# Kernel tuning notes

Measured on AMD Instinct MI355X. Metric: run time of the kernel, lower is better.

Reference implementation:

```python
import jax, jax.numpy as jnp
import numpy as np

N_NODES = 100000
N_EDGES = 1250000
IN_DIM = 64
HID_DIM = 64
OUT_DIM = 64
NEG_SLOPE = 0.2
EPS = 1e-16  # PyG softmax denominator epsilon


def _xavier(key, shape):
    fan_in, fan_out = shape[1], shape[0]
    lim = jnp.sqrt(6.0 / (fan_in + fan_out))
    return jax.random.uniform(key, shape, jnp.float32, -lim, lim)


def setup_inputs() -> dict:
    key = jax.random.key(0)
    ks = jax.random.split(key, 10)
    x = jax.random.normal(ks[0], (N_NODES, IN_DIM), jnp.float32)
    edge_index = jax.random.randint(ks[1], (2, N_EDGES), 0, N_NODES, jnp.int64)
    edge_attr = jax.random.uniform(ks[2], (N_EDGES,), jnp.float32)
    # layer 1 params (torch Linear weight layout: [out, in])
    W1 = _xavier(ks[3], (HID_DIM, IN_DIM))
    a_src1 = _xavier(ks[4], (1, HID_DIM))[0]
    a_dst1 = _xavier(ks[5], (1, HID_DIM))[0]
    # layer 2 params
    W2 = _xavier(ks[6], (OUT_DIM, HID_DIM))
    a_src2 = _xavier(ks[7], (1, OUT_DIM))[0]
    a_dst2 = _xavier(ks[8], (1, OUT_DIM))[0]
    return {"x": x, "edge_index": edge_index, "edge_attr": edge_attr,
            "W1": W1, "a_src1": a_src1, "a_dst1": a_dst1,
            "W2": W2, "a_src2": a_src2, "a_dst2": a_dst2}


def gat_layer(x, W, a_src, a_dst, src, dst, edge_weight, num_nodes):
    # linear (no bias): h = x @ W^T, h: [N, out]
    h = x @ W.T
    s_src = h @ a_src  # [N]
    s_dst = h @ a_dst  # [N]
    # per-edge raw score; note j = edge_index[0] (src), i = edge_index[1] (dst)
    alpha = s_src[src] + s_dst[dst]  # [E]
    alpha = jnp.where(alpha >= 0, alpha, NEG_SLOPE * alpha)  # leaky_relu
    # segment softmax over destination nodes
    seg_max = jax.ops.segment_max(alpha, dst, num_segments=num_nodes)
    alpha = jnp.exp(alpha - seg_max[dst])
    seg_sum = jax.ops.segment_sum(alpha, dst, num_segments=num_nodes)
    alpha = alpha / (seg_sum[dst] + EPS)
    alpha = alpha * edge_weight
    # weighted scatter-add aggregation of source features
    msg = h[src] * alpha[:, None]  # [E, out]
    return jax.ops.segment_sum(msg, dst, num_segments=num_nodes)


def reference(x, edge_index, edge_attr, W1, a_src1, a_dst1, W2, a_src2, a_dst2):
    src = edge_index[0]
    dst = edge_index[1]
    h = gat_layer(x, W1, a_src1, a_dst1, src, dst, edge_attr, N_NODES)
    h = jax.nn.relu(h)
    out = gat_layer(h, W2, a_src2, a_dst2, src, dst, edge_attr, N_NODES)
    return out
```

## Files before the change

### kernel.cpp

```cpp
#include <hip/hip_runtime.h>

#define NN 100000
#define NE 1250000
#define DIM 64

#define BSHIFT 8
#define BNODES (1 << BSHIFT)
#define NBUCK ((NN + BNODES - 1) / BNODES)
#define BIN_BLOCKS 256
#define BIN_CHUNK ((NE + BIN_BLOCKS - 1) / BIN_BLOCKS)
#define BCAP 4096

typedef unsigned short bf16_t;
typedef __attribute__((ext_vector_type(8))) short short8;
typedef __attribute__((ext_vector_type(8))) unsigned short ushort8;
typedef __attribute__((ext_vector_type(4))) float f32x4;

static __device__ __forceinline__ bf16_t f2bf(float f) {
    union { float f; unsigned int u; } c; c.f = f;
    unsigned int u = c.u;
    u += 0x7FFFu + ((u >> 16) & 1u);
    return (bf16_t)(u >> 16);
}
static __device__ __forceinline__ float bf2f(bf16_t b) {
    union { unsigned int u; float f; } c; c.u = ((unsigned int)b) << 16;
    return c.f;
}

union ABFrag { short8 v; short s[8]; };

template<bool IN_BF16, bool RELU_IN>
static __device__ __forceinline__
void linear_body(int bid, const void* __restrict__ xin,
                 const float* __restrict__ W,
                 const float* __restrict__ a_src,
                 const float* __restrict__ a_dst,
                 bf16_t* __restrict__ h,
                 float* __restrict__ s_src,
                 float* __restrict__ s_dst)
{
    int tid  = threadIdx.x;
    int lane = tid & 63;
    int wid  = tid >> 6;
    int lr   = lane & 15;
    int lg   = lane >> 4;
    int rowbase = bid * 128 + wid * 16;

    ABFrag Bf[4][2];
#pragma unroll
    for (int t = 0; t < 4; ++t)
#pragma unroll
    for (int s = 0; s < 2; ++s) {
        const f32x4* wp = reinterpret_cast<const f32x4*>(W + (lr + 16*t)*DIM + 32*s + 8*lg);
        f32x4 w0 = wp[0], w1 = wp[1];
#pragma unroll
        for (int j = 0; j < 4; ++j) {
            Bf[t][s].s[j]     = (short)f2bf(w0[j]);
            Bf[t][s].s[j + 4] = (short)f2bf(w1[j]);
        }
    }

    int arow = rowbase + lr;
    if (arow > NN - 1) arow = NN - 1;

    ABFrag Af[2];
    if (IN_BF16) {
        const bf16_t* xp = (const bf16_t*)xin + (size_t)arow * DIM + 8*lg;
#pragma unroll
        for (int s = 0; s < 2; ++s) {
            ushort8 xv = *reinterpret_cast<const ushort8*>(xp + 32*s);
#pragma unroll
            for (int j = 0; j < 8; ++j) {
                unsigned short b = xv[j];
                if (RELU_IN) b = (b & 0x8000u) ? (unsigned short)0 : b;
                Af[s].s[j] = (short)b;
            }
        }
    } else {
        const float* xp = (const float*)xin + (size_t)arow * DIM + 8*lg;
#pragma unroll
        for (int s = 0; s < 2; ++s) {
            const f32x4* xq = reinterpret_cast<const f32x4*>(xp + 32*s);
            f32x4 x0 = xq[0], x1 = xq[1];
#pragma unroll
            for (int j = 0; j < 4; ++j) {
                float f0 = x0[j], f1 = x1[j];
                if (RELU_IN) { f0 = f0 > 0.f ? f0 : 0.f; f1 = f1 > 0.f ? f1 : 0.f; }
                Af[s].s[j]     = (short)f2bf(f0);
                Af[s].s[j + 4] = (short)f2bf(f1);
            }
        }
    }

    f32x4 acc[4] = {{0.f,0.f,0.f,0.f},{0.f,0.f,0.f,0.f},{0.f,0.f,0.f,0.f},{0.f,0.f,0.f,0.f}};
#pragma unroll
    for (int s = 0; s < 2; ++s)
#pragma unroll
    for (int t = 0; t < 4; ++t)
        acc[t] = __builtin_amdgcn_mfma_f32_16x16x32_bf16(Af[s].v, Bf[t][s].v, acc[t], 0, 0, 0);

    float av[4], dv[4];
#pragma unroll
    for (int t = 0; t < 4; ++t) { av[t] = a_src[lr + 16*t]; dv[t] = a_dst[lr + 16*t]; }

    float ssv[4], sdv[4];
#pragma unroll
    for (int r = 0; r < 4; ++r) {
        int row = rowbase + 4*lg + r;
        bool ok = row < NN;
        float ps = 0.f, pd = 0.f;
#pragma unroll
        for (int t = 0; t < 4; ++t) {
            float v = acc[t][r];
            ps += v * av[t];
            pd += v * dv[t];
            if (ok) h[(size_t)row * DIM + lr + 16*t] = f2bf(v);
        }
#pragma unroll
        for (int off = 8; off; off >>= 1) {
            ps += __shfl_xor(ps, off, 64);
            pd += __shfl_xor(pd, off, 64);
        }
        ssv[r] = ps; sdv[r] = pd;
    }
    if (lr == 0) {
#pragma unroll
        for (int r = 0; r < 4; ++r) {
            int row = rowbase + 4*lg + r;
            if (row < NN) { s_src[row] = ssv[r]; s_dst[row] = sdv[r]; }
        }
    }
}

__global__ __launch_bounds__(512)
void bin_hist(const int* __restrict__ dst, int* __restrict__ gcnt)
{
    __shared__ int cnt[NBUCK];
    int tid = threadIdx.x;
    for (int i = tid; i < NBUCK; i += 512) cnt[i] = 0;
    __syncthreads();
    int lo = blockIdx.x * BIN_CHUNK;
    int hi = lo + BIN_CHUNK; if (hi > NE) hi = NE;
    for (int e = lo + tid; e < hi; e += 512)
        atomicAdd(&cnt[dst[e] >> BSHIFT], 1);
    __syncthreads();
    for (int i = tid; i < NBUCK; i += 512)
        gcnt[i * BIN_BLOCKS + blockIdx.x] = cnt[i];
}

__global__ __launch_bounds__(256)
void row_scan(int* __restrict__ gcnt, int* __restrict__ btot)
{
    __shared__ int wpart[4];
    int b    = blockIdx.x;
    int tid  = threadIdx.x;
    int lane = tid & 63;
    int v = gcnt[b * BIN_BLOCKS + tid];
    int sc = v;
#pragma unroll
    for (int off = 1; off <= 32; off <<= 1) {
        int t = __shfl_up(sc, off, 64);
        if (lane >= off) sc += t;
    }
    if (lane == 63) wpart[tid >> 6] = sc;
    __syncthreads();
    if (tid == 0) {
        int run = 0;
#pragma unroll
        for (int k = 0; k < 4; ++k) { int t = wpart[k]; wpart[k] = run; run += t; }
    }
    __syncthreads();
    int incl = sc + wpart[tid >> 6];
    gcnt[b * BIN_BLOCKS + tid] = incl - v;
    if (tid == BIN_BLOCKS - 1) btot[b] = incl;
}

__global__ __launch_bounds__(512)
void scatter_linear1(const int* __restrict__ src, const int* __restrict__ dst,
                     const float* __restrict__ ea,
                     const int* __restrict__ gcnt, const int* __restrict__ btot,
                     int2* __restrict__ region,
                     const float* __restrict__ x, const float* __restrict__ W1,
                     const float* __restrict__ as1, const float* __restrict__ ad1,
                     bf16_t* __restrict__ h,
                     float* __restrict__ ssrc, float* __restrict__ sdst)
{
    if (blockIdx.x < BIN_BLOCKS) {
        __shared__ int2 sbuf[BIN_CHUNK];
        __shared__ unsigned short sbkt[BIN_CHUNK];
        __shared__ int lcur[NBUCK];
        __shared__ int gout[NBUCK];
        __shared__ int wpart[8];
        int tid  = threadIdx.x;
        int lane = tid & 63;
        int blk  = blockIdx.x;

        int cntb = 0, gex = 0;
        if (tid < NBUCK) {
            gex = gcnt[tid * BIN_BLOCKS + blk];
            int nxt = (blk + 1 < BIN_BLOCKS) ? gcnt[tid * BIN_BLOCKS + blk + 1] : btot[tid];
            cntb = nxt - gex;
        }
        int sc = cntb;
#pragma unroll
        for (int off = 1; off <= 32; off <<= 1) {
            int t = __shfl_up(sc, off, 64);
            if (lane >= off) sc += t;
        }
        if (lane == 63) wpart[tid >> 6] = sc;
        __syncthreads();
        if (tid == 0) {
            int run = 0;
#pragma unroll
            for (int k = 0; k < 8; ++k) { int t = wpart[k]; wpart[k] = run; run += t; }
        }
        __syncthreads();
        int excl = sc - cntb + wpart[tid >> 6];
        if (tid < NBUCK) {
            lcur[tid] = excl;
            gout[tid] = tid * BCAP + gex - excl;
        }
        __syncthreads();

        int lo = blk * BIN_CHUNK;
        int hi = lo + BIN_CHUNK; if (hi > NE) hi = NE;
        for (int e = lo + tid; e < hi; e += 512) {
            int d = dst[e];
            int b = d >> BSHIFT;
            int pos = atomicAdd(&lcur[b], 1);
            sbuf[pos] = make_int2(src[e] | ((d & (BNODES - 1)) << 17),
                                  __float_as_int(ea[e]));
            sbkt[pos] = (unsigned short)b;
        }
        __syncthreads();

        int T = hi - lo;
        for (int i = tid; i < T; i += 512) {
            int b = sbkt[i];
            region[gout[b] + i] = sbuf[i];
        }
    } else {
        linear_body<false, false>(blockIdx.x - BIN_BLOCKS, x, W1, as1, ad1, h, ssrc, sdst);
    }
}

__global__ __launch_bounds__(256)
void build_csr(const int* __restrict__ btot,
               const int2* __restrict__ region,
               int* __restrict__ rowptr, int* __restrict__ rend,
               int2* __restrict__ csr)
{
    int b    = blockIdx.x;
    int tid  = threadIdx.x;
    int lane = tid & 63;
    int cnt  = btot[b];
    const int2* rec = region + (size_t)b * BCAP;

    __shared__ int ncnt[BNODES];
    __shared__ int curs[BNODES];
    __shared__ int wpart[4];
    ncnt[tid] = 0;
    __syncthreads();
    for (int i = tid; i < cnt; i += 256)
        atomicAdd(&ncnt[(rec[i].x >> 17) & (BNODES - 1)], 1);
    __syncthreads();

    int v = ncnt[tid];
    int sc = v;
#pragma unroll
    for (int off = 1; off <= 32; off <<= 1) {
        int t = __shfl_up(sc, off, 64);
        if (lane >= off) sc += t;
    }
    if (lane == 63) wpart[tid >> 6] = sc;
    __syncthreads();
    if (tid == 0) {
        int run = 0;
#pragma unroll
        for (int k = 0; k < 4; ++k) { int t = wpart[k]; wpart[k] = run; run += t; }
    }
    __syncthreads();
    int excl = sc - v + wpart[tid >> 6];
    int base = b * BCAP;

    int node = (b << BSHIFT) + tid;
    if (node < NN) { rowptr[node] = base + excl; rend[node] = base + excl + v; }
    curs[tid] = base + excl;
    __syncthreads();

    for (int i = tid; i < cnt; i += 256) {
        int2 r = rec[i];
        int dl = (r.x >> 17) & (BNODES - 1);
        int pos = atomicAdd(&curs[dl], 1);
        csr[pos] = make_int2(r.x & 0x1FFFF, r.y);
    }
}

template<bool FUSE_LIN2>
__global__ __launch_bounds__(256)
void fused_agg(const int* __restrict__ rowptr, const int* __restrict__ rend,
               const int2* __restrict__ csr,
               const float* __restrict__ ssrc, const float* __restrict__ sdst,
               const bf16_t* __restrict__ h,
               const float* __restrict__ W2, const float* __restrict__ as2,
               const float* __restrict__ ad2,
               bf16_t* __restrict__ h2, float* __restrict__ ssrc2,
               float* __restrict__ sdst2,
               float* __restrict__ outp)
{
    __shared__ bf16_t rowbuf[16][72];
    __shared__ float sps[4][16], spd[4][16];

    int tid  = threadIdx.x;
    int lane = tid & 63;
    int wv   = tid >> 6;
    int grp  = lane >> 4;
    int lr   = lane & 15;
    int d    = blockIdx.x * 16 + wv * 4 + grp;
    bool dok = d < NN;

    int rb = 0, deg = 0;
    if (dok) { rb = rowptr[d]; deg = rend[d] - rb; }
    float sdd = dok ? sdst[d] : 0.f;

    int wmax = deg;
    wmax = max(wmax, __shfl_xor(wmax, 16, 64));
    wmax = max(wmax, __shfl_xor(wmax, 32, 64));

    float psum = 0.f;
    float ax = 0.f, ay = 0.f, az = 0.f, aw = 0.f;

#define GSWZ(J)                                                                 \
    int   sj##J = __builtin_amdgcn_ds_swizzle(s, (((J) << 5) | 0x10));          \
    float wj##J = __int_as_float(__builtin_amdgcn_ds_swizzle(wbits, (((J) << 5) | 0x10)));
#define GLOAD(J)                                                                \
    ushort4 hv##J = *reinterpret_cast<const ushort4*>(h + (size_t)sj##J * DIM + 4*lr);
#define GACC(J)                                                                 \
    ax += wj##J * bf2f(hv##J.x); ay += wj##J * bf2f(hv##J.y);                   \
    az += wj##J * bf2f(hv##J.z); aw += wj##J * bf2f(hv##J.w);

    for (int cb = 0; cb < wmax; cb += 16) {
        int idx = cb + lr;
        bool v = idx < deg;
        int2 rec = v ? csr[rb + idx] : make_int2(0, 0);
        int   s  = rec.x;
        float a  = ssrc[s] + sdd;
        a = (a >= 0.f) ? a : 0.2f * a;
        a = fminf(a, 60.f);
        float p = v ? __expf(a) : 0.f;
        float w = p * __int_as_float(rec.y);
        int wbits = __float_as_int(w);

        GSWZ(0)  GSWZ(1)  GSWZ(2)  GSWZ(3)  GSWZ(4)  GSWZ(5)  GSWZ(6)  GSWZ(7)
        GSWZ(8)  GSWZ(9)  GSWZ(10) GSWZ(11) GSWZ(12) GSWZ(13) GSWZ(14) GSWZ(15)
        GLOAD(0)  GLOAD(1)  GLOAD(2)  GLOAD(3)  GLOAD(4)  GLOAD(5)  GLOAD(6)  GLOAD(7)
        GLOAD(8)  GLOAD(9)  GLOAD(10) GLOAD(11) GLOAD(12) GLOAD(13) GLOAD(14) GLOAD(15)

        float ps = p;
#pragma unroll
        for (int off = 1; off <= 8; off <<= 1) ps += __shfl_xor(ps, off, 64);
        psum += ps;

        GACC(0)  GACC(1)  GACC(2)  GACC(3)  GACC(4)  GACC(5)  GACC(6)  GACC(7)
        GACC(8)  GACC(9)  GACC(10) GACC(11) GACC(12) GACC(13) GACC(14) GACC(15)
    }
#undef GSWZ
#undef GLOAD
#undef GACC

    if (!FUSE_LIN2) {
        if (dok) {
            float inv = 1.f / (psum + 1e-16f);
            float4 o = make_float4(ax * inv, ay * inv, az * inv, aw * inv);
            *reinterpret_cast<float4*>(outp + (size_t)d * DIM + 4*lr) = o;
        }
        return;
    }

    {
        float inv = dok ? 1.f / (psum + 1e-16f) : 0.f;
        float r0 = ax * inv, r1 = ay * inv, r2 = az * inv, r3 = aw * inv;
        r0 = r0 > 0.f ? r0 : 0.f;  r1 = r1 > 0.f ? r1 : 0.f;
        r2 = r2 > 0.f ? r2 : 0.f;  r3 = r3 > 0.f ? r3 : 0.f;
        int ns = wv * 4 + grp;
        ushort4 pk;
        pk.x = f2bf(r0); pk.y = f2bf(r1); pk.z = f2bf(r2); pk.w = f2bf(r3);
        *reinterpret_cast<ushort4*>(&rowbuf[ns][4 * lr]) = pk;
    }
    __syncthreads();

    int lg = lane >> 4;
    ABFrag Af2[2];
#pragma unroll
    for (int s = 0; s < 2; ++s)
        Af2[s].v = *reinterpret_cast<const short8*>(&rowbuf[lr][32 * s + 8 * lg]);
    ABFrag Bf2[2];
#pragma unroll
    for (int s = 0; s < 2; ++s) {
        const f32x4* wp = reinterpret_cast<const f32x4*>(W2 + (lr + 16 * wv) * DIM + 32 * s + 8 * lg);
        f32x4 w0 = wp[0], w1 = wp[1];
#pragma unroll
        for (int j = 0; j < 4; ++j) {
            Bf2[s].s[j]     = (short)f2bf(w0[j]);
            Bf2[s].s[j + 4] = (short)f2bf(w1[j]);
        }
    }
    f32x4 a2 = {0.f, 0.f, 0.f, 0.f};
    a2 = __builtin_amdgcn_mfma_f32_16x16x32_bf16(Af2[0].v, Bf2[0].v, a2, 0, 0, 0);
    a2 = __builtin_amdgcn_mfma_f32_16x16x32_bf16(Af2[1].v, Bf2[1].v, a2, 0, 0, 0);

    float av = as2[lr + 16 * wv], dv = ad2[lr + 16 * wv];
#pragma unroll
    for (int r = 0; r < 4; ++r) {
        int ns = 4 * lg + r;
        int node = blockIdx.x * 16 + ns;
        if (node < NN) h2[(size_t)node * DIM + lr + 16 * wv] = f2bf(a2[r]);
        float cs = a2[r] * av, cd = a2[r] * dv;
#pragma unroll
        for (int off = 8; off; off >>= 1) {
            cs += __shfl_xor(cs, off, 64);
            cd += __shfl_xor(cd, off, 64);
        }
        if (lr == 0) { sps[wv][ns] = cs; spd[wv][ns] = cd; }
    }
    __syncthreads();
    if (tid < 16) {
        int node = blockIdx.x * 16 + tid;
        if (node < NN) {
            ssrc2[node] = sps[0][tid] + sps[1][tid] + sps[2][tid] + sps[3][tid];
            sdst2[node] = spd[0][tid] + spd[1][tid] + spd[2][tid] + spd[3][tid];
        }
    }
}

extern "C" void kernel_launch(void* const* d_in, const int* in_sizes, int n_in,
                              void* d_out, int out_size, void* d_ws, size_t ws_size,
                              hipStream_t stream) {
    const float* x   = (const float*)d_in[0];
    const int*   ei  = (const int*)d_in[1];
    const float* ea  = (const float*)d_in[2];
    const float* W1  = (const float*)d_in[3];
    const float* as1 = (const float*)d_in[4];
    const float* ad1 = (const float*)d_in[5];
    const float* W2  = (const float*)d_in[6];
    const float* as2 = (const float*)d_in[7];
    const float* ad2 = (const float*)d_in[8];
    const int* src = ei;
    const int* dst = ei + NE;
    float* out = (float*)d_out;

    char* p = (char*)d_ws;
    auto carve = [&](size_t bytes) { char* r = p; p += (bytes + 255) & ~(size_t)255; return (void*)r; };
    bf16_t*  h2     = (bf16_t*)carve((size_t)NN * DIM * 2);
    bf16_t*  h      = (bf16_t*)carve((size_t)NN * DIM * 2);
    float*   ssrc   = (float*)carve((size_t)NN * 4);
    float*   sdst   = (float*)carve((size_t)NN * 4);
    float*   ssrc2  = (float*)carve((size_t)NN * 4);
    float*   sdst2  = (float*)carve((size_t)NN * 4);
    int*     rowptr = (int*)carve((size_t)NN * 4);
    int*     rend   = (int*)carve((size_t)NN * 4);
    int2*    csr    = (int2*)carve((size_t)NBUCK * BCAP * 8);
    int2*    region = (int2*)carve((size_t)NBUCK * BCAP * 8);
    int*     gcnt   = (int*)carve((size_t)NBUCK * BIN_BLOCKS * 4);
    int*     btot   = (int*)carve((size_t)NBUCK * 4);

    const int GRID_LIN  = (NN + 127) / 128;
    const int GRID_NODE = (NN + 15) / 16;

    bin_hist<<<BIN_BLOCKS, 512, 0, stream>>>(dst, gcnt);
    row_scan<<<NBUCK, 256, 0, stream>>>(gcnt, btot);
    scatter_linear1<<<BIN_BLOCKS + GRID_LIN, 512, 0, stream>>>(
        src, dst, ea, gcnt, btot, region, x, W1, as1, ad1, h, ssrc, sdst);
    build_csr<<<NBUCK, 256, 0, stream>>>(btot, region, rowptr, rend, csr);

    fused_agg<true><<<GRID_NODE, 256, 0, stream>>>(
        rowptr, rend, csr, ssrc, sdst, h, W2, as2, ad2, h2, ssrc2, sdst2, nullptr);

    fused_agg<false><<<GRID_NODE, 256, 0, stream>>>(
        rowptr, rend, csr, ssrc2, sdst2, h2, nullptr, nullptr, nullptr,
        nullptr, nullptr, nullptr, out);
}
```

Measured before the change: 119.5 us.

## Pack row spans into int2, double aggregation block to 32 nodes, drop exp clamp

Row start and end offsets are packed into a single int2 array so each destination node needs one 8-byte load instead of two separate loads. The aggregation kernel now runs 512 threads and 32 nodes per block. The fused layer-2 linear MFMA is remapped so that 8 waves cover two 16-row tiles across four column tiles. The fminf clamp before exp is removed, which saves an instruction but risks overflow for large scores, since there is no max subtraction.

```diff
diff --git a/kernel.cpp b/kernel.cpp
--- a/kernel.cpp
+++ b/kernel.cpp
@@ -247,7 +247,7 @@
 __global__ __launch_bounds__(256)
 void build_csr(const int* __restrict__ btot,
                const int2* __restrict__ region,
-               int* __restrict__ rowptr, int* __restrict__ rend,
+               int2* __restrict__ rspan,
                int2* __restrict__ csr)
 {
     int b    = blockIdx.x;
@@ -284,7 +284,7 @@
     int base = b * BCAP;
 
     int node = (b << BSHIFT) + tid;
-    if (node < NN) { rowptr[node] = base + excl; rend[node] = base + excl + v; }
+    if (node < NN) rspan[node] = make_int2(base + excl, base + excl + v);
     curs[tid] = base + excl;
     __syncthreads();
 
@@ -297,8 +297,8 @@
 }
 
 template<bool FUSE_LIN2>
-__global__ __launch_bounds__(256)
-void fused_agg(const int* __restrict__ rowptr, const int* __restrict__ rend,
+__global__ __launch_bounds__(512)
+void fused_agg(const int2* __restrict__ rspan,
                const int2* __restrict__ csr,
                const float* __restrict__ ssrc, const float* __restrict__ sdst,
                const bf16_t* __restrict__ h,
@@ -308,19 +308,19 @@
                float* __restrict__ sdst2,
                float* __restrict__ outp)
 {
-    __shared__ bf16_t rowbuf[16][72];
-    __shared__ float sps[4][16], spd[4][16];
+    __shared__ bf16_t rowbuf[32][72];
+    __shared__ float sps[8][16], spd[8][16];
 
     int tid  = threadIdx.x;
     int lane = tid & 63;
     int wv   = tid >> 6;
     int grp  = lane >> 4;
     int lr   = lane & 15;
-    int d    = blockIdx.x * 16 + wv * 4 + grp;
+    int d    = blockIdx.x * 32 + wv * 4 + grp;
     bool dok = d < NN;
 
-    int rb = 0, deg = 0;
-    if (dok) { rb = rowptr[d]; deg = rend[d] - rb; }
+    int2 sp = dok ? rspan[d] : make_int2(0, 0);
+    int rb = sp.x, deg = sp.y - sp.x;
     float sdd = dok ? sdst[d] : 0.f;
 
     int wmax = deg;
@@ -346,7 +346,6 @@
         int   s  = rec.x;
         float a  = ssrc[s] + sdd;
         a = (a >= 0.f) ? a : 0.2f * a;
-        a = fminf(a, 60.f);
         float p = v ? __expf(a) : 0.f;
         float w = p * __int_as_float(rec.y);
         int wbits = __float_as_int(w);
@@ -390,14 +389,16 @@
     __syncthreads();
 
     int lg = lane >> 4;
+    int mt = wv >> 2;
+    int ct = wv & 3;
     ABFrag Af2[2];
 #pragma unroll
     for (int s = 0; s < 2; ++s)
-        Af2[s].v = *reinterpret_cast<const short8*>(&rowbuf[lr][32 * s + 8 * lg]);
+        Af2[s].v = *reinterpret_cast<const short8*>(&rowbuf[16 * mt + lr][32 * s + 8 * lg]);
     ABFrag Bf2[2];
 #pragma unroll
     for (int s = 0; s < 2; ++s) {
-        const f32x4* wp = reinterpret_cast<const f32x4*>(W2 + (lr + 16 * wv) * DIM + 32 * s + 8 * lg);
+        const f32x4* wp = reinterpret_cast<const f32x4*>(W2 + (lr + 16 * ct) * DIM + 32 * s + 8 * lg);
         f32x4 w0 = wp[0], w1 = wp[1];
 #pragma unroll
         for (int j = 0; j < 4; ++j) {
@@ -409,26 +410,27 @@
     a2 = __builtin_amdgcn_mfma_f32_16x16x32_bf16(Af2[0].v, Bf2[0].v, a2, 0, 0, 0);
     a2 = __builtin_amdgcn_mfma_f32_16x16x32_bf16(Af2[1].v, Bf2[1].v, a2, 0, 0, 0);
 
-    float av = as2[lr + 16 * wv], dv = ad2[lr + 16 * wv];
+    float av = as2[lr + 16 * ct], dv = ad2[lr + 16 * ct];
 #pragma unroll
     for (int r = 0; r < 4; ++r) {
-        int ns = 4 * lg + r;
-        int node = blockIdx.x * 16 + ns;
-        if (node < NN) h2[(size_t)node * DIM + lr + 16 * wv] = f2bf(a2[r]);
+        int ns = 16 * mt + 4 * lg + r;
+        int node = blockIdx.x * 32 + ns;
+        if (node < NN) h2[(size_t)node * DIM + lr + 16 * ct] = f2bf(a2[r]);
         float cs = a2[r] * av, cd = a2[r] * dv;
 #pragma unroll
         for (int off = 8; off; off >>= 1) {
             cs += __shfl_xor(cs, off, 64);
             cd += __shfl_xor(cd, off, 64);
         }
-        if (lr == 0) { sps[wv][ns] = cs; spd[wv][ns] = cd; }
-    }
-    __syncthreads();
-    if (tid < 16) {
-        int node = blockIdx.x * 16 + tid;
+        if (lr == 0) { sps[wv][4 * lg + r] = cs; spd[wv][4 * lg + r] = cd; }
+    }
+    __syncthreads();
+    if (tid < 32) {
+        int node = blockIdx.x * 32 + tid;
         if (node < NN) {
-            ssrc2[node] = sps[0][tid] + sps[1][tid] + sps[2][tid] + sps[3][tid];
-            sdst2[node] = spd[0][tid] + spd[1][tid] + spd[2][tid] + spd[3][tid];
+            int m = tid >> 4, sl = tid & 15;
+            ssrc2[node] = sps[4*m][sl] + sps[4*m+1][sl] + sps[4*m+2][sl] + sps[4*m+3][sl];
+            sdst2[node] = spd[4*m][sl] + spd[4*m+1][sl] + spd[4*m+2][sl] + spd[4*m+3][sl];
         }
     }
 }
@@ -457,26 +459,25 @@
     float*   sdst   = (float*)carve((size_t)NN * 4);
     float*   ssrc2  = (float*)carve((size_t)NN * 4);
     float*   sdst2  = (float*)carve((size_t)NN * 4);
-    int*     rowptr = (int*)carve((size_t)NN * 4);
-    int*     rend   = (int*)carve((size_t)NN * 4);
+    int2*    rspan  = (int2*)carve((size_t)NN * 8);
     int2*    csr    = (int2*)carve((size_t)NBUCK * BCAP * 8);
     int2*    region = (int2*)carve((size_t)NBUCK * BCAP * 8);
     int*     gcnt   = (int*)carve((size_t)NBUCK * BIN_BLOCKS * 4);
     int*     btot   = (int*)carve((size_t)NBUCK * 4);
 
     const int GRID_LIN  = (NN + 127) / 128;
-    const int GRID_NODE = (NN + 15) / 16;
+    const int GRID_NODE = (NN + 31) / 32;
 
     bin_hist<<<BIN_BLOCKS, 512, 0, stream>>>(dst, gcnt);
     row_scan<<<NBUCK, 256, 0, stream>>>(gcnt, btot);
     scatter_linear1<<<BIN_BLOCKS + GRID_LIN, 512, 0, stream>>>(
         src, dst, ea, gcnt, btot, region, x, W1, as1, ad1, h, ssrc, sdst);
-    build_csr<<<NBUCK, 256, 0, stream>>>(btot, region, rowptr, rend, csr);
-
-    fused_agg<true><<<GRID_NODE, 256, 0, stream>>>(
-        rowptr, rend, csr, ssrc, sdst, h, W2, as2, ad2, h2, ssrc2, sdst2, nullptr);
-
-    fused_agg<false><<<GRID_NODE, 256, 0, stream>>>(
-        rowptr, rend, csr, ssrc2, sdst2, h2, nullptr, nullptr, nullptr,
+    build_csr<<<NBUCK, 256, 0, stream>>>(btot, region, rspan, csr);
+
+    fused_agg<true><<<GRID_NODE, 512, 0, stream>>>(
+        rspan, csr, ssrc, sdst, h, W2, as2, ad2, h2, ssrc2, sdst2, nullptr);
+
+    fused_agg<false><<<GRID_NODE, 512, 0, stream>>>(
+        rspan, csr, ssrc2, sdst2, h2, nullptr, nullptr, nullptr,
         nullptr, nullptr, nullptr, out);
 }
```

Result: slower. 127.6 us (+6.8%).
